# Kernel optimization log

Hardware: AMD Instinct MI355X
Metric: run time of the kernel (lower is better)

Reference implementation:

```python
import jax, jax.numpy as jnp
import numpy as np

N = 100000   # nodes
E = 1600000  # edges
F = 128      # input features
H = 128      # hidden channels
G = 64       # graphs in batch
EPS = 1e-5   # BatchNorm eps


def setup_inputs() -> dict:
    key = jax.random.key(0)
    ks = jax.random.split(key, 24)
    s = 0.05
    d = {}
    d["x"] = jax.random.normal(ks[0], (N, F), jnp.float32)
    d["edge_index"] = jax.random.randint(ks[1], (2, E), 0, N, dtype=jnp.int32)
    d["batch"] = jnp.sort(jax.random.randint(ks[2], (N,), 0, G, dtype=jnp.int32))
    # GCNConv weights/biases
    d["W1"] = jax.random.normal(ks[3], (F, H), jnp.float32) * s
    d["b1"] = jnp.zeros((H,), jnp.float32)
    d["W2"] = jax.random.normal(ks[4], (H, H), jnp.float32) * s
    d["b2"] = jnp.zeros((H,), jnp.float32)
    d["W3"] = jax.random.normal(ks[5], (H, H), jnp.float32) * s
    d["b3"] = jnp.zeros((H,), jnp.float32)
    # BatchNorm affine params
    for i, k in zip((1, 2, 3), (ks[6], ks[7], ks[8])):
        d[f"g{i}"] = jnp.ones((H,), jnp.float32) + jax.random.normal(k, (H,), jnp.float32) * 0.01
        d[f"be{i}"] = jnp.zeros((H,), jnp.float32)
    # MLP: Linear(2H, H) -> ReLU -> Linear(H, 1)
    d["Wm1"] = jax.random.normal(ks[9], (2 * H, H), jnp.float32) * s
    d["bm1"] = jnp.zeros((H,), jnp.float32)
    d["Wm2"] = jax.random.normal(ks[10], (H, 1), jnp.float32) * s
    d["bm2"] = jnp.zeros((1,), jnp.float32)
    return d


def _gcn_conv(x, W, b, src, dst, dinv):
    # PyG GCNConv: h = D^{-1/2}(A+I)D^{-1/2} (x W) + b, with self-loops
    h = x @ W                                   # [N, H]
    norm = (dinv[src] * dinv[dst])[:, None]     # [E, 1]
    agg = jax.ops.segment_sum(h[src] * norm, dst, num_segments=N)
    agg = agg + h * (dinv * dinv)[:, None]      # self-loop term
    return agg + b


def _bn(x, g, be):
    # BatchNorm1d, training-mode batch stats (biased variance), over node dim
    m = jnp.mean(x, axis=0)
    v = jnp.var(x, axis=0)
    return (x - m) * jax.lax.rsqrt(v + EPS) * g + be


def reference(x, W1, b1, g1, be1, W2, b2, g2, be2, W3, b3, g3, be3,
              Wm1, bm1, Wm2, bm2, edge_index, batch):
    src, dst = edge_index[0], edge_index[1]
    # degree with self-loops (edge weight 1)
    deg = jax.ops.segment_sum(jnp.ones((E,), x.dtype), dst, num_segments=N) + 1.0
    dinv = jax.lax.rsqrt(deg)

    h = jax.nn.relu(_bn(_gcn_conv(x, W1, b1, src, dst, dinv), g1, be1))  # dropout(p=0.05) = identity in eval
    res = h
    h = jax.nn.relu(_bn(_gcn_conv(h, W2, b2, src, dst, dinv), g2, be2)) + res
    res = h
    h = jax.nn.relu(_bn(_gcn_conv(h, W3, b3, src, dst, dinv), g3, be3)) + res

    x_sum = jax.ops.segment_sum(h, batch, num_segments=G)                 # [G, H]
    cnt = jax.ops.segment_sum(jnp.ones((N,), h.dtype), batch, num_segments=G)
    x_mean = x_sum / jnp.maximum(cnt, 1.0)[:, None]
    z = jnp.concatenate([x_sum, x_mean], axis=-1)                         # [G, 2H]
    z = jax.nn.relu(z @ Wm1 + bm1)
    return z @ Wm2 + bm2                                                  # [G, 1]
```

## Files before the change

kernel.cpp:

```cpp
#include <hip/hip_runtime.h>

#define NN 100000
#define EE 1600000
#define HD 128
#define GG 64
#define NB 391
#define BNEPS 1e-5f

typedef unsigned int uint_t;
typedef unsigned short ushort_t;

static __device__ __forceinline__ ushort_t f2bf(float f){
  uint_t b = __float_as_uint(f);
  return (ushort_t)((b + 0x7FFFu + ((b >> 16) & 1u)) >> 16);
}
static __device__ __forceinline__ uint_t pack2bf(float a, float b){
  return (uint_t)f2bf(a) | ((uint_t)f2bf(b) << 16);
}
static __device__ __forceinline__ float bflo(uint_t u){ return __uint_as_float(u << 16); }
static __device__ __forceinline__ float bfhi(uint_t u){ return __uint_as_float(u & 0xFFFF0000u); }

__global__ void k_hist(const int* __restrict__ ei, int* __restrict__ cnt){
  int e = blockIdx.x*256 + threadIdx.x;
  if (e < EE) atomicAdd(&cnt[ei[EE + e]], 1);
}

__global__ void k_dinv(const int* __restrict__ cnt, float* __restrict__ dinv){
  int n = blockIdx.x*256 + threadIdx.x;
  if (n < NN) dinv[n] = rsqrtf(1.0f + (float)cnt[n]);
}

__global__ void k_scanA(const int* __restrict__ cnt, int* __restrict__ offs,
                        int* __restrict__ bsum){
  __shared__ int s[256];
  int tid = threadIdx.x;
  int n = blockIdx.x*256 + tid;
  int v = (n < NN) ? cnt[n] : 0;
  s[tid] = v; __syncthreads();
  for (int d = 1; d < 256; d <<= 1){
    int t = (tid >= d) ? s[tid-d] : 0;
    __syncthreads();
    s[tid] += t;
    __syncthreads();
  }
  if (n < NN) offs[n] = s[tid] - v;
  if (tid == 255) bsum[blockIdx.x] = s[255];
}

__global__ void k_scanB(int* __restrict__ bsum){
  __shared__ int s[512];
  int tid = threadIdx.x;
  int v = (tid < NB) ? bsum[tid] : 0;
  s[tid] = v; __syncthreads();
  for (int d = 1; d < 512; d <<= 1){
    int t = (tid >= d) ? s[tid-d] : 0;
    __syncthreads();
    s[tid] += t;
    __syncthreads();
  }
  if (tid < NB) bsum[tid] = s[tid] - v;
}

__global__ void k_scanC(int* __restrict__ offs, const int* __restrict__ bsum){
  int n = blockIdx.x*256 + threadIdx.x;
  if (n < NN) offs[n] += bsum[blockIdx.x];
  if (n == 0) offs[NN] = EE;
}

__global__ void k_scatter(const int* __restrict__ ei, const int* __restrict__ offs,
                          int* __restrict__ cursor, const float* __restrict__ dinv,
                          int2* __restrict__ csr){
  int e = blockIdx.x*256 + threadIdx.x;
  if (e >= EE) return;
  int s = ei[e], d = ei[EE + e];
  int pos = offs[d] + atomicAdd(&cursor[d], 1);
  csr[pos] = make_int2(s, __float_as_int(dinv[s]));
}

__global__ void __launch_bounds__(256)
k_agg(const ushort_t* __restrict__ hb, const int2* __restrict__ csr,
      const int* __restrict__ offs, const float* __restrict__ dinv,
      const float* __restrict__ bias, float* __restrict__ agg,
      float* __restrict__ bns){
  const int wib  = threadIdx.x >> 6;
  const int lane = threadIdx.x & 63;
  const int gw = blockIdx.x*4 + wib;
  const int nw = gridDim.x*4;
  const int c0 = lane*2;
  const float2 b2 = *(const float2*)&bias[c0];
  float sx=0.f, sy=0.f, qx=0.f, qy=0.f;
  for (int n = gw; n < NN; n += nw){
    const float dn = dinv[n];
    const uint_t hv = *(const uint_t*)&hb[(size_t)n*HD + c0];
    float ax = bflo(hv)*dn, ay = bfhi(hv)*dn;
    const int b0 = offs[n], b1 = offs[n+1];
    int e = b0;
    for (; e + 8 <= b1; e += 8){
      const int2 p0 = csr[e+0];
      const int2 p1 = csr[e+1];
      const int2 p2 = csr[e+2];
      const int2 p3 = csr[e+3];
      const int2 p4 = csr[e+4];
      const int2 p5 = csr[e+5];
      const int2 p6 = csr[e+6];
      const int2 p7 = csr[e+7];
      const uint_t u0 = *(const uint_t*)&hb[(size_t)p0.x*HD + c0];
      const uint_t u1 = *(const uint_t*)&hb[(size_t)p1.x*HD + c0];
      const uint_t u2 = *(const uint_t*)&hb[(size_t)p2.x*HD + c0];
      const uint_t u3 = *(const uint_t*)&hb[(size_t)p3.x*HD + c0];
      const uint_t u4 = *(const uint_t*)&hb[(size_t)p4.x*HD + c0];
      const uint_t u5 = *(const uint_t*)&hb[(size_t)p5.x*HD + c0];
      const uint_t u6 = *(const uint_t*)&hb[(size_t)p6.x*HD + c0];
      const uint_t u7 = *(const uint_t*)&hb[(size_t)p7.x*HD + c0];
      const float w0 = __int_as_float(p0.y), w1 = __int_as_float(p1.y);
      const float w2 = __int_as_float(p2.y), w3 = __int_as_float(p3.y);
      const float w4 = __int_as_float(p4.y), w5 = __int_as_float(p5.y);
      const float w6 = __int_as_float(p6.y), w7 = __int_as_float(p7.y);
      ax = fmaf(bflo(u0), w0, ax); ay = fmaf(bfhi(u0), w0, ay);
      ax = fmaf(bflo(u1), w1, ax); ay = fmaf(bfhi(u1), w1, ay);
      ax = fmaf(bflo(u2), w2, ax); ay = fmaf(bfhi(u2), w2, ay);
      ax = fmaf(bflo(u3), w3, ax); ay = fmaf(bfhi(u3), w3, ay);
      ax = fmaf(bflo(u4), w4, ax); ay = fmaf(bfhi(u4), w4, ay);
      ax = fmaf(bflo(u5), w5, ax); ay = fmaf(bfhi(u5), w5, ay);
      ax = fmaf(bflo(u6), w6, ax); ay = fmaf(bfhi(u6), w6, ay);
      ax = fmaf(bflo(u7), w7, ax); ay = fmaf(bfhi(u7), w7, ay);
    }
    for (; e + 4 <= b1; e += 4){
      const int2 p0 = csr[e+0];
      const int2 p1 = csr[e+1];
      const int2 p2 = csr[e+2];
      const int2 p3 = csr[e+3];
      const uint_t u0 = *(const uint_t*)&hb[(size_t)p0.x*HD + c0];
      const uint_t u1 = *(const uint_t*)&hb[(size_t)p1.x*HD + c0];
      const uint_t u2 = *(const uint_t*)&hb[(size_t)p2.x*HD + c0];
      const uint_t u3 = *(const uint_t*)&hb[(size_t)p3.x*HD + c0];
      const float w0 = __int_as_float(p0.y), w1 = __int_as_float(p1.y);
      const float w2 = __int_as_float(p2.y), w3 = __int_as_float(p3.y);
      ax = fmaf(bflo(u0), w0, ax); ay = fmaf(bfhi(u0), w0, ay);
      ax = fmaf(bflo(u1), w1, ax); ay = fmaf(bfhi(u1), w1, ay);
      ax = fmaf(bflo(u2), w2, ax); ay = fmaf(bfhi(u2), w2, ay);
      ax = fmaf(bflo(u3), w3, ax); ay = fmaf(bfhi(u3), w3, ay);
    }
    for (; e < b1; ++e){
      const int2 p = csr[e];
      const float w = __int_as_float(p.y);
      const uint_t u = *(const uint_t*)&hb[(size_t)p.x*HD + c0];
      ax = fmaf(bflo(u), w, ax);
      ay = fmaf(bfhi(u), w, ay);
    }
    const float ox = fmaf(ax, dn, b2.x);
    const float oy = fmaf(ay, dn, b2.y);
    *(float2*)&agg[(size_t)n*HD + c0] = make_float2(ox, oy);
    sx += ox; sy += oy; qx += ox*ox; qy += oy*oy;
  }
  __shared__ float red[4][64][4];
  red[wib][lane][0]=sx; red[wib][lane][1]=sy; red[wib][lane][2]=qx; red[wib][lane][3]=qy;
  __syncthreads();
  if (wib == 0){
    float a0=0.f,a1=0.f,a2=0.f,a3=0.f;
    #pragma unroll
    for (int w=0; w<4; ++w){
      a0+=red[w][lane][0]; a1+=red[w][lane][1]; a2+=red[w][lane][2]; a3+=red[w][lane][3];
    }
    atomicAdd(&bns[c0  ],    a0);
    atomicAdd(&bns[c0+1],    a1);
    atomicAdd(&bns[HD+c0  ], a2);
    atomicAdd(&bns[HD+c0+1], a3);
  }
}

__global__ void k_bnfin(const float* __restrict__ bns, const float* __restrict__ g,
                        const float* __restrict__ be, float* __restrict__ scale,
                        float* __restrict__ shift){
  int c = threadIdx.x;
  float m = bns[c] * (1.0f/NN);
  float v = bns[HD+c] * (1.0f/NN) - m*m;
  float sc = g[c] * rsqrtf(v + BNEPS);
  scale[c] = sc;
  shift[c] = be[c] - m*sc;
}

template<int MODE>
__global__ void __launch_bounds__(256)
k_rowgemm(const float* __restrict__ A, const float* __restrict__ res,
          const float* __restrict__ W, const float* __restrict__ scale,
          const float* __restrict__ shift,
          ushort_t* __restrict__ HB, float* __restrict__ HOUT){
  __shared__ float Wl[32*128];
  __shared__ float At[32*68];
  const int tid = threadIdx.x;
  const int n0 = blockIdx.x*64;
  const int tx = tid & 31;
  const int ty = tid >> 5;
  float4 acc[8];
  #pragma unroll
  for (int i=0;i<8;i++) acc[i] = make_float4(0.f,0.f,0.f,0.f);

  for (int kk=0; kk<128; kk+=32){
    #pragma unroll
    for (int p=0;p<4;p++){
      int idx = tid*4 + p*1024;
      *(float4*)&Wl[idx] = *(const float4*)&W[kk*128 + idx];
    }
    #pragma unroll
    for (int p=0;p<2;p++){
      int idx = tid*4 + p*1024;
      int r = idx >> 5;
      int c = idx & 31;
      int n = n0 + r;
      float4 v = make_float4(0.f,0.f,0.f,0.f);
      if (n < NN){
        v = *(const float4*)&A[(size_t)n*HD + kk + c];
        if (MODE >= 1){
          const float4 sc = *(const float4*)&scale[kk+c];
          const float4 sh = *(const float4*)&shift[kk+c];
          v.x = fmaxf(fmaf(v.x, sc.x, sh.x), 0.f);
          v.y = fmaxf(fmaf(v.y, sc.y, sh.y), 0.f);
          v.z = fmaxf(fmaf(v.z, sc.z, sh.z), 0.f);
          v.w = fmaxf(fmaf(v.w, sc.w, sh.w), 0.f);
          if (MODE == 2){
            const float4 rv = *(const float4*)&res[(size_t)n*HD + kk + c];
            v.x += rv.x; v.y += rv.y; v.z += rv.z; v.w += rv.w;
          }
          *(float4*)&HOUT[(size_t)n*HD + kk + c] = v;
        }
      }
      At[(c+0)*68 + r] = v.x;
      At[(c+1)*68 + r] = v.y;
      At[(c+2)*68 + r] = v.z;
      At[(c+3)*68 + r] = v.w;
    }
    __syncthreads();
    #pragma unroll 8
    for (int k=0;k<32;k++){
      const float4 b  = *(const float4*)&Wl[k*128 + tx*4];
      const float4 a0 = *(const float4*)&At[k*68 + ty*8];
      const float4 a1 = *(const float4*)&At[k*68 + ty*8 + 4];
      const float av[8] = {a0.x,a0.y,a0.z,a0.w,a1.x,a1.y,a1.z,a1.w};
      #pragma unroll
      for (int i=0;i<8;i++){
        acc[i].x = fmaf(av[i], b.x, acc[i].x);
        acc[i].y = fmaf(av[i], b.y, acc[i].y);
        acc[i].z = fmaf(av[i], b.z, acc[i].z);
        acc[i].w = fmaf(av[i], b.w, acc[i].w);
      }
    }
    __syncthreads();
  }
  #pragma unroll
  for (int i=0;i<8;i++){
    int n = n0 + ty*8 + i;
    if (n < NN){
      *(uint2*)&HB[(size_t)n*HD + tx*4] =
        make_uint2(pack2bf(acc[i].x, acc[i].y), pack2bf(acc[i].z, acc[i].w));
    }
  }
}

__global__ void __launch_bounds__(128)
k_pool(const float* __restrict__ agg, const float* __restrict__ scale,
       const float* __restrict__ shift, const float* __restrict__ h2,
       const int* __restrict__ batch, float* __restrict__ pool,
       float* __restrict__ pcnt){
  const int t = threadIdx.x;
  const int n0 = blockIdx.x*128;
  const float sc = scale[t], sh = shift[t];
  float racc = 0.f;
  int cur = -1, runlen = 0;
  for (int i=0;i<128;i++){
    int n = n0 + i;
    if (n >= NN) break;
    int g = batch[n];
    float v = fmaxf(fmaf(agg[(size_t)n*HD + t], sc, sh), 0.f) + h2[(size_t)n*HD + t];
    if (g != cur){
      if (cur >= 0){
        atomicAdd(&pool[cur*HD + t], racc);
        if (t == 0) atomicAdd(&pcnt[cur], (float)runlen);
      }
      cur = g; racc = 0.f; runlen = 0;
    }
    racc += v; runlen++;
  }
  if (cur >= 0){
    atomicAdd(&pool[cur*HD + t], racc);
    if (t == 0) atomicAdd(&pcnt[cur], (float)runlen);
  }
}

__global__ void __launch_bounds__(128)
k_mlp(const float* __restrict__ pool, const float* __restrict__ pcnt,
      const float* __restrict__ Wm1, const float* __restrict__ bm1,
      const float* __restrict__ Wm2, const float* __restrict__ bm2,
      float* __restrict__ out){
  __shared__ float z[2*HD];
  __shared__ float red[HD];
  const int g = blockIdx.x, t = threadIdx.x;
  float s = pool[g*HD + t];
  float c = fmaxf(pcnt[g], 1.0f);
  z[t] = s; z[HD + t] = s / c;
  __syncthreads();
  float acc = bm1[t];
  for (int i=0;i<2*HD;i++) acc = fmaf(z[i], Wm1[i*HD + t], acc);
  acc = fmaxf(acc, 0.f);
  red[t] = acc * Wm2[t];
  __syncthreads();
  for (int off=64; off>0; off>>=1){
    if (t < off) red[t] += red[t+off];
    __syncthreads();
  }
  if (t == 0) out[g] = red[0] + bm2[0];
}

extern "C" void kernel_launch(void* const* d_in, const int* in_sizes, int n_in,
                              void* d_out, int out_size, void* d_ws, size_t ws_size,
                              hipStream_t stream){
  const float* x   = (const float*)d_in[0];
  const int*  ei   = (const int*)d_in[1];
  const int*  batch= (const int*)d_in[2];
  const float* W1  = (const float*)d_in[3];
  const float* b1  = (const float*)d_in[4];
  const float* W2  = (const float*)d_in[5];
  const float* b2  = (const float*)d_in[6];
  const float* W3  = (const float*)d_in[7];
  const float* b3  = (const float*)d_in[8];
  const float* g1  = (const float*)d_in[9];
  const float* be1 = (const float*)d_in[10];
  const float* g2  = (const float*)d_in[11];
  const float* be2 = (const float*)d_in[12];
  const float* g3  = (const float*)d_in[13];
  const float* be3 = (const float*)d_in[14];
  const float* Wm1 = (const float*)d_in[15];
  const float* bm1 = (const float*)d_in[16];
  const float* Wm2 = (const float*)d_in[17];
  const float* bm2 = (const float*)d_in[18];
  float* out = (float*)d_out;
  (void)in_sizes; (void)n_in; (void)out_size; (void)ws_size;

  char* p = (char*)d_ws;
  auto alloc = [&](size_t bytes)->void*{
    void* r = (void*)p;
    p += (bytes + 511) & ~(size_t)511;
    return r;
  };
  int*   deg    = (int*)  alloc(NN*sizeof(int));
  int*   cursor = (int*)  alloc(NN*sizeof(int));
  float* bns    = (float*)alloc(3*2*HD*sizeof(float));
  float* pool   = (float*)alloc(GG*HD*sizeof(float));
  float* pcnt   = (float*)alloc(GG*sizeof(float));
  size_t zbytes = (size_t)(p - (char*)d_ws);
  int*   offs   = (int*)  alloc((NN+1)*sizeof(int));
  int*   bsum   = (int*)  alloc(512*sizeof(int));
  float* dinv   = (float*)alloc(NN*sizeof(float));
  float* scale  = (float*)alloc(3*HD*sizeof(float));
  float* shift  = (float*)alloc(3*HD*sizeof(float));
  int2*  csr    = (int2*) alloc(((size_t)EE+8)*sizeof(int2));
  ushort_t* hb  = (ushort_t*)alloc((size_t)NN*HD*sizeof(ushort_t));
  float* agg    = (float*)alloc((size_t)NN*HD*sizeof(float));
  float* hres   = (float*)alloc((size_t)NN*HD*sizeof(float));

  hipMemsetAsync(d_ws, 0, zbytes, stream);

  k_hist   <<<(EE+255)/256, 256, 0, stream>>>(ei, deg);
  k_dinv   <<<NB, 256, 0, stream>>>(deg, dinv);
  k_scanA  <<<NB, 256, 0, stream>>>(deg, offs, bsum);
  k_scanB  <<<1, 512, 0, stream>>>(bsum);
  k_scanC  <<<NB, 256, 0, stream>>>(offs, bsum);
  k_scatter<<<(EE+255)/256, 256, 0, stream>>>(ei, offs, cursor, dinv, csr);

  const int GB = (NN+63)/64;
  k_rowgemm<0><<<GB, 256, 0, stream>>>(x,   nullptr, W1, nullptr,    nullptr,    hb, nullptr);
  k_agg       <<<2048, 256, 0, stream>>>(hb, csr, offs, dinv, b1, agg, bns);
  k_bnfin     <<<1, 128, 0, stream>>>(bns,        g1, be1, scale,      shift);
  k_rowgemm<1><<<GB, 256, 0, stream>>>(agg, nullptr, W2, scale,      shift,      hb, hres);
  k_agg       <<<2048, 256, 0, stream>>>(hb, csr, offs, dinv, b2, agg, bns + 2*HD);
  k_bnfin     <<<1, 128, 0, stream>>>(bns + 2*HD, g2, be2, scale+HD,   shift+HD);
  k_rowgemm<2><<<GB, 256, 0, stream>>>(agg, hres,    W3, scale+HD,   shift+HD,   hb, hres);
  k_agg       <<<2048, 256, 0, stream>>>(hb, csr, offs, dinv, b3, agg, bns + 4*HD);
  k_bnfin     <<<1, 128, 0, stream>>>(bns + 4*HD, g3, be3, scale+2*HD, shift+2*HD);

  k_pool<<<(NN+127)/128, 128, 0, stream>>>(agg, scale+2*HD, shift+2*HD, hres, batch, pool, pcnt);
  k_mlp <<<GG, 128, 0, stream>>>(pool, pcnt, Wm1, bm1, Wm2, bm2, out);
}
```

Baseline: 951.6 us.

## Use bf16 MFMA for row GEMMs with pre-transposed bf16 weights

Replaces the fp32 FMA tiled GEMM in k_rowgemm with bf16 MFMA 16x16x32 instructions. The activation tile is staged in LDS as bf16 and the weights come from a transposed bf16 copy built by a new small conversion kernel. The goal is to cut ALU time in the three feature transforms. The cost is bf16 rounding of the GEMM inputs and three extra tiny launches. It also folds the dinv computation into the scan kernel, which removes one launch.

New measurement: 976.3 us. 1.03x slower.

```diff
diff --git a/kernel.cpp b/kernel.cpp
--- a/kernel.cpp
+++ b/kernel.cpp
@@ -9,6 +9,8 @@
 
 typedef unsigned int uint_t;
 typedef unsigned short ushort_t;
+typedef __attribute__((ext_vector_type(8))) short bf16x8;
+typedef __attribute__((ext_vector_type(4))) float f32x4;
 
 static __device__ __forceinline__ ushort_t f2bf(float f){
   uint_t b = __float_as_uint(f);
@@ -25,17 +27,13 @@
   if (e < EE) atomicAdd(&cnt[ei[EE + e]], 1);
 }
 
-__global__ void k_dinv(const int* __restrict__ cnt, float* __restrict__ dinv){
-  int n = blockIdx.x*256 + threadIdx.x;
-  if (n < NN) dinv[n] = rsqrtf(1.0f + (float)cnt[n]);
-}
-
 __global__ void k_scanA(const int* __restrict__ cnt, int* __restrict__ offs,
-                        int* __restrict__ bsum){
+                        int* __restrict__ bsum, float* __restrict__ dinv){
   __shared__ int s[256];
   int tid = threadIdx.x;
   int n = blockIdx.x*256 + tid;
   int v = (n < NN) ? cnt[n] : 0;
+  if (n < NN) dinv[n] = rsqrtf(1.0f + (float)v);
   s[tid] = v; __syncthreads();
   for (int d = 1; d < 256; d <<= 1){
     int t = (tid >= d) ? s[tid-d] : 0;
@@ -75,6 +73,11 @@
   int s = ei[e], d = ei[EE + e];
   int pos = offs[d] + atomicAdd(&cursor[d], 1);
   csr[pos] = make_int2(s, __float_as_int(dinv[s]));
+}
+
+__global__ void k_wconv(const float* __restrict__ W, ushort_t* __restrict__ Wt){
+  const int c = blockIdx.x, k = threadIdx.x;
+  Wt[c*HD + k] = f2bf(W[k*HD + c]);
 }
 
 __global__ void __launch_bounds__(256)
@@ -183,76 +186,74 @@
 template<int MODE>
 __global__ void __launch_bounds__(256)
 k_rowgemm(const float* __restrict__ A, const float* __restrict__ res,
-          const float* __restrict__ W, const float* __restrict__ scale,
+          const ushort_t* __restrict__ Wt, const float* __restrict__ scale,
           const float* __restrict__ shift,
           ushort_t* __restrict__ HB, float* __restrict__ HOUT){
-  __shared__ float Wl[32*128];
-  __shared__ float At[32*68];
-  const int tid = threadIdx.x;
-  const int n0 = blockIdx.x*64;
-  const int tx = tid & 31;
-  const int ty = tid >> 5;
-  float4 acc[8];
-  #pragma unroll
-  for (int i=0;i<8;i++) acc[i] = make_float4(0.f,0.f,0.f,0.f);
-
-  for (int kk=0; kk<128; kk+=32){
-    #pragma unroll
-    for (int p=0;p<4;p++){
-      int idx = tid*4 + p*1024;
-      *(float4*)&Wl[idx] = *(const float4*)&W[kk*128 + idx];
-    }
-    #pragma unroll
-    for (int p=0;p<2;p++){
-      int idx = tid*4 + p*1024;
-      int r = idx >> 5;
-      int c = idx & 31;
-      int n = n0 + r;
-      float4 v = make_float4(0.f,0.f,0.f,0.f);
-      if (n < NN){
-        v = *(const float4*)&A[(size_t)n*HD + kk + c];
+  __shared__ ushort_t Al[64][136];
+  const int tid  = threadIdx.x;
+  const int wv   = tid >> 6;
+  const int lane = tid & 63;
+  const int n0   = blockIdx.x * 64;
+
+  {
+    const int r = tid >> 2;
+    const int q = tid & 3;
+    const int n = n0 + r;
+    const int cb = q*32;
+    uint_t pk[16];
+    if (n < NN){
+      #pragma unroll
+      for (int j=0;j<8;j++){
+        float4 v = *(const float4*)&A[(size_t)n*HD + cb + j*4];
         if (MODE >= 1){
-          const float4 sc = *(const float4*)&scale[kk+c];
-          const float4 sh = *(const float4*)&shift[kk+c];
+          const float4 sc = *(const float4*)&scale[cb + j*4];
+          const float4 sh = *(const float4*)&shift[cb + j*4];
           v.x = fmaxf(fmaf(v.x, sc.x, sh.x), 0.f);
           v.y = fmaxf(fmaf(v.y, sc.y, sh.y), 0.f);
           v.z = fmaxf(fmaf(v.z, sc.z, sh.z), 0.f);
           v.w = fmaxf(fmaf(v.w, sc.w, sh.w), 0.f);
           if (MODE == 2){
-            const float4 rv = *(const float4*)&res[(size_t)n*HD + kk + c];
+            const float4 rv = *(const float4*)&res[(size_t)n*HD + cb + j*4];
             v.x += rv.x; v.y += rv.y; v.z += rv.z; v.w += rv.w;
           }
-          *(float4*)&HOUT[(size_t)n*HD + kk + c] = v;
+          *(float4*)&HOUT[(size_t)n*HD + cb + j*4] = v;
         }
+        pk[2*j]   = pack2bf(v.x, v.y);
+        pk[2*j+1] = pack2bf(v.z, v.w);
       }
-      At[(c+0)*68 + r] = v.x;
-      At[(c+1)*68 + r] = v.y;
-      At[(c+2)*68 + r] = v.z;
-      At[(c+3)*68 + r] = v.w;
-    }
-    __syncthreads();
-    #pragma unroll 8
-    for (int k=0;k<32;k++){
-      const float4 b  = *(const float4*)&Wl[k*128 + tx*4];
-      const float4 a0 = *(const float4*)&At[k*68 + ty*8];
-      const float4 a1 = *(const float4*)&At[k*68 + ty*8 + 4];
-      const float av[8] = {a0.x,a0.y,a0.z,a0.w,a1.x,a1.y,a1.z,a1.w};
+    } else {
       #pragma unroll
-      for (int i=0;i<8;i++){
-        acc[i].x = fmaf(av[i], b.x, acc[i].x);
-        acc[i].y = fmaf(av[i], b.y, acc[i].y);
-        acc[i].z = fmaf(av[i], b.z, acc[i].z);
-        acc[i].w = fmaf(av[i], b.w, acc[i].w);
-      }
-    }
-    __syncthreads();
-  }
+      for (int i=0;i<16;i++) pk[i] = 0;
+    }
+    #pragma unroll
+    for (int i=0;i<4;i++)
+      *(uint4*)&Al[r][cb + i*8] = *(const uint4*)&pk[i*4];
+  }
+  __syncthreads();
+
+  const int mrow = wv*16 + (lane & 15);
+  const int kg8  = (lane >> 4) * 8;
+  const int bcol = lane & 15;
+  f32x4 acc[8];
   #pragma unroll
-  for (int i=0;i<8;i++){
-    int n = n0 + ty*8 + i;
-    if (n < NN){
-      *(uint2*)&HB[(size_t)n*HD + tx*4] =
-        make_uint2(pack2bf(acc[i].x, acc[i].y), pack2bf(acc[i].z, acc[i].w));
+  for (int t=0;t<8;t++) acc[t] = (f32x4){0.f,0.f,0.f,0.f};
+  #pragma unroll
+  for (int ks=0; ks<4; ks++){
+    const bf16x8 af = *(const bf16x8*)&Al[mrow][ks*32 + kg8];
+    #pragma unroll
+    for (int ct=0; ct<8; ct++){
+      const bf16x8 bf = *(const bf16x8*)&Wt[(size_t)(ct*16 + bcol)*HD + ks*32 + kg8];
+      acc[ct] = __builtin_amdgcn_mfma_f32_16x16x32_bf16(af, bf, acc[ct], 0, 0, 0);
+    }
+  }
+
+  const int drow = wv*16 + ((lane >> 4) << 2);
+  #pragma unroll
+  for (int ct=0; ct<8; ct++){
+    #pragma unroll
+    for (int r=0; r<4; r++){
+      const int n = n0 + drow + r;
+      if (n < NN) HB[(size_t)n*HD + ct*16 + bcol] = f2bf(acc[ct][r]);
     }
   }
 }
@@ -353,6 +354,9 @@
   float* dinv   = (float*)alloc(NN*sizeof(float));
   float* scale  = (float*)alloc(3*HD*sizeof(float));
   float* shift  = (float*)alloc(3*HD*sizeof(float));
+  ushort_t* wt1 = (ushort_t*)alloc(HD*HD*sizeof(ushort_t));
+  ushort_t* wt2 = (ushort_t*)alloc(HD*HD*sizeof(ushort_t));
+  ushort_t* wt3 = (ushort_t*)alloc(HD*HD*sizeof(ushort_t));
   int2*  csr    = (int2*) alloc(((size_t)EE+8)*sizeof(int2));
   ushort_t* hb  = (ushort_t*)alloc((size_t)NN*HD*sizeof(ushort_t));
   float* agg    = (float*)alloc((size_t)NN*HD*sizeof(float));
@@ -361,20 +365,22 @@
   hipMemsetAsync(d_ws, 0, zbytes, stream);
 
   k_hist   <<<(EE+255)/256, 256, 0, stream>>>(ei, deg);
-  k_dinv   <<<NB, 256, 0, stream>>>(deg, dinv);
-  k_scanA  <<<NB, 256, 0, stream>>>(deg, offs, bsum);
+  k_scanA  <<<NB, 256, 0, stream>>>(deg, offs, bsum, dinv);
   k_scanB  <<<1, 512, 0, stream>>>(bsum);
   k_scanC  <<<NB, 256, 0, stream>>>(offs, bsum);
   k_scatter<<<(EE+255)/256, 256, 0, stream>>>(ei, offs, cursor, dinv, csr);
+  k_wconv  <<<HD, HD, 0, stream>>>(W1, wt1);
+  k_wconv  <<<HD, HD, 0, stream>>>(W2, wt2);
+  k_wconv  <<<HD, HD, 0, stream>>>(W3, wt3);
 
   const int GB = (NN+63)/64;
-  k_rowgemm<0><<<GB, 256, 0, stream>>>(x,   nullptr, W1, nullptr,    nullptr,    hb, nullptr);
+  k_rowgemm<0><<<GB, 256, 0, stream>>>(x,   nullptr, wt1, nullptr,    nullptr,    hb, nullptr);
   k_agg       <<<2048, 256, 0, stream>>>(hb, csr, offs, dinv, b1, agg, bns);
   k_bnfin     <<<1, 128, 0, stream>>>(bns,        g1, be1, scale,      shift);
-  k_rowgemm<1><<<GB, 256, 0, stream>>>(agg, nullptr, W2, scale,      shift,      hb, hres);
+  k_rowgemm<1><<<GB, 256, 0, stream>>>(agg, nullptr, wt2, scale,      shift,      hb, hres);
   k_agg       <<<2048, 256, 0, stream>>>(hb, csr, offs, dinv, b2, agg, bns + 2*HD);
   k_bnfin     <<<1, 128, 0, stream>>>(bns + 2*HD, g2, be2, scale+HD,   shift+HD);
-  k_rowgemm<2><<<GB, 256, 0, stream>>>(agg, hres,    W3, scale+HD,   shift+HD,   hb, hres);
+  k_rowgemm<2><<<GB, 256, 0, stream>>>(agg, hres,    wt3, scale+HD,   shift+HD,   hb, hres);
   k_agg       <<<2048, 256, 0, stream>>>(hb, csr, offs, dinv, b3, agg, bns + 4*HD);
   k_bnfin     <<<1, 128, 0, stream>>>(bns + 4*HD, g3, be3, scale+2*HD, shift+2*HD);
 
```
